# Optimization experiments

Hardware: AMD Instinct MI355X
Metric: run time of the kernel (lower is better)

Reference implementation:

```python
import jax, jax.numpy as jnp
import numpy as np

B, S, D = 2, 2048, 1024   # batch, seq, d_model
E, K, H = 8, 4, 1024      # experts, top-k, expert hidden
SH = 2 * H                # shared-expert hidden (n_shared_experts=2)


def setup_inputs() -> dict:
    key = jax.random.key(0)
    ks = jax.random.split(key, 24)
    f = lambda k, shape: jax.random.normal(k, shape, dtype=jnp.float32) * 0.02
    return {
        "x": jax.random.normal(ks[0], (B, S, D), dtype=jnp.float32),
        # Linear(in_features, out_features), stored as [in, out]
        "lin0_w": f(ks[1], (D, D)), "lin0_b": f(ks[2], (D,)),
        "swi1_w1": f(ks[3], (D, D)), "swi1_b1": f(ks[4], (D,)),
        "swi1_w2": f(ks[5], (D, D)), "swi1_b2": f(ks[6], (D,)),
        # MoE router (no bias) + routed experts (SwiGLU FFN, no bias)
        "gate_w": f(ks[7], (E, D)),
        "exp_w1": f(ks[8], (E, D, H)),
        "exp_w3": f(ks[9], (E, D, H)),
        "exp_w2": f(ks[10], (E, H, D)),
        # shared experts fused into one wider SwiGLU MLP (2 shared experts)
        "sh_w1": f(ks[11], (D, SH)),
        "sh_w3": f(ks[12], (D, SH)),
        "sh_w2": f(ks[13], (SH, D)),
        # second Linear + SwiGLU block (num_ff=2)
        "lin1_w": f(ks[14], (D, D)), "lin1_b": f(ks[15], (D,)),
        "swi2_w1": f(ks[16], (D, D)), "swi2_b1": f(ks[17], (D,)),
        "swi2_w2": f(ks[18], (D, D)), "swi2_b2": f(ks[19], (D,)),
    }


def _silu(x):
    return x * jax.nn.sigmoid(x)


def _swiglu(x, w1, b1, w2, b2):
    return _silu(x @ w1 + b1) * (x @ w2 + b2)


def _moe(x, gate_w, exp_w1, exp_w3, exp_w2, sh_w1, sh_w3, sh_w2):
    b, s, d = x.shape
    t = b * s
    xt = x.reshape(t, d)
    # router: softmax scores, greedy top-k, normalized weights (scaling factor = 1)
    scores = jax.nn.softmax(xt @ gate_w.T, axis=-1)          # [T, E]
    topv, topi = jax.lax.top_k(scores, K)                    # [T, K]
    topv = topv / jnp.sum(topv, axis=-1, keepdims=True)
    combine = jnp.zeros((t, E), xt.dtype).at[jnp.arange(t)[:, None], topi].set(topv)  # [T, E]
    # routed experts: SwiGLU FFN per expert, dense-masked combine (same math as dispatch)
    g = _silu(jnp.einsum('td,edh->eth', xt, exp_w1))
    u = jnp.einsum('td,edh->eth', xt, exp_w3)
    yexp = jnp.einsum('eth,ehd->etd', g * u, exp_w2)         # [E, T, D]
    routed = jnp.einsum('te,etd->td', combine, yexp)         # [T, D]
    # shared experts (always on)
    shared = (_silu(xt @ sh_w1) * (xt @ sh_w3)) @ sh_w2      # [T, D]
    return (routed + shared).reshape(b, s, d)


def reference(x, lin0_w, lin0_b, swi1_w1, swi1_b1, swi1_w2, swi1_b2,
              gate_w, exp_w1, exp_w3, exp_w2, sh_w1, sh_w3, sh_w2,
              lin1_w, lin1_b, swi2_w1, swi2_b1, swi2_w2, swi2_b2):
    h = x @ lin0_w + lin0_b
    h = _swiglu(h, swi1_w1, swi1_b1, swi1_w2, swi1_b2)
    h = _moe(h, gate_w, exp_w1, exp_w3, exp_w2, sh_w1, sh_w3, sh_w2)
    h = h @ lin1_w + lin1_b
    h = _swiglu(h, swi2_w1, swi2_b1, swi2_w2, swi2_b2)
    return h
```

## Files before the change

kernel.cpp:

```cpp
#include <hip/hip_runtime.h>
#include <cstdint>
#include <cstddef>

#define T_TOKENS 4096
#define D_MODEL  1024
#define N_EXP    8
#define TOP_K    4
#define H_EXP    1024
#define SH_HID   2048
#define TK       (T_TOKENS*TOP_K)

typedef __bf16 bf16x8 __attribute__((ext_vector_type(8)));
typedef __bf16 bf16x4 __attribute__((ext_vector_type(4)));
typedef float  f32x4  __attribute__((ext_vector_type(4)));

__device__ __forceinline__ float silu_f(float x) {
    return x / (1.0f + expf(-x));
}

template<int NT, bool SEG, bool GATHER, bool GLU>
__global__ __launch_bounds__(256)
void gemm_sp(const float* __restrict__ A, int lda,
             const float* __restrict__ W1, const float* __restrict__ W3,
             int64_t w_estride, int ldw,
             const float* __restrict__ bias1, const float* __restrict__ bias2,
             float* __restrict__ C, __bf16* __restrict__ Cb1, int ldc,
             int M, int Kd,
             const int* __restrict__ seg_off,
             const int* __restrict__ gather)
{
    constexpr int BM = 128, BN = 128, BK = 32;
    __shared__ __bf16 Asl[NT][BM * BK];
    __shared__ __bf16 Bsl[NT][BN * BK];

    int m0, m1, e = 0;
    if (SEG) {
        e = blockIdx.z;
        int s0 = seg_off[e], s1 = seg_off[e + 1];
        m0 = s0 + blockIdx.y * BM;
        if (m0 >= s1) return;
        m1 = (m0 + BM < s1) ? (m0 + BM) : s1;
    } else {
        m0 = blockIdx.y * BM;
        m1 = (m0 + BM < M) ? (m0 + BM) : M;
    }
    const int n0 = blockIdx.x * BN;

    const int tid  = threadIdx.x;
    const int lane = tid & 63;
    const int w    = tid >> 6;
    const int wm   = w >> 1, wn = w & 1;
    const int fr   = lane & 15, fq = lane >> 4;

    const float* aP[4]; int aR[4], aQ[4];
#pragma unroll
    for (int i = 0; i < 4; ++i) {
        int Li = tid + 256 * i;
        int r = Li >> 3, q = Li & 7;
        aR[i] = r; aQ[i] = q;
        int grow = m0 + r;
        if (grow > m1 - 1) grow = m1 - 1;
        if (GATHER) grow = gather[grow];
        aP[i] = A + (int64_t)grow * lda + q * 4;
    }

    const int bn  = tid & 127;
    const int bkh = tid >> 7;
    const float* Wsrc; int wcol;
    if (GLU) {
        int cl = n0 + bn;
        int B  = cl >> 4;
        Wsrc = (B & 1) ? W3 : W1;
        wcol = ((B >> 1) << 4) | (cl & 15);
    } else {
        Wsrc = W1; wcol = n0 + bn;
    }
    const float* Wb = Wsrc + (int64_t)e * w_estride + (int64_t)(bkh * 16) * ldw + wcol;

    f32x4 zero4 = {0.f, 0.f, 0.f, 0.f};
    f32x4 acc[4][4];
#pragma unroll
    for (int i = 0; i < 4; ++i)
#pragma unroll
        for (int j = 0; j < 4; ++j) acc[i][j] = zero4;

    float4 av[4];
    float  wv[16];

#define GLOADS(K0)                                                         \
    do {                                                                   \
        _Pragma("unroll")                                                  \
        for (int i = 0; i < 4; ++i)                                        \
            av[i] = *reinterpret_cast<const float4*>(aP[i] + (K0));        \
        _Pragma("unroll")                                                  \
        for (int j = 0; j < 16; ++j)                                       \
            wv[j] = Wb[(int64_t)((K0) + j) * ldw];                         \
    } while (0)

    const int nk = Kd / BK;
    GLOADS(0);

    for (int ks = 0; ks < nk; ++ks) {
        bf16x4 pa[NT][4];
        bf16x4 pw[NT][4];
#pragma unroll
        for (int i = 0; i < 4; ++i) {
            float vv[4] = {av[i].x, av[i].y, av[i].z, av[i].w};
#pragma unroll
            for (int t = 0; t < 4; ++t) {
                float v = vv[t];
                __bf16 h = (__bf16)v;
                pa[0][i][t] = h;
                if (NT >= 2) {
                    float r = v - (float)h;
                    if (NT == 2) {
                        pa[1][i][t] = (__bf16)r;
                    } else {
                        __bf16 m = (__bf16)r;
                        pa[1][i][t] = m;
                        pa[2][i][t] = (__bf16)(r - (float)m);
                    }
                }
            }
        }
#pragma unroll
        for (int qd = 0; qd < 4; ++qd) {
#pragma unroll
            for (int t = 0; t < 4; ++t) {
                float v = wv[qd * 4 + t];
                __bf16 h = (__bf16)v;
                pw[0][qd][t] = h;
                if (NT >= 2) {
                    float r = v - (float)h;
                    if (NT == 2) {
                        pw[1][qd][t] = (__bf16)r;
                    } else {
                        __bf16 m = (__bf16)r;
                        pw[1][qd][t] = m;
                        pw[2][qd][t] = (__bf16)(r - (float)m);
                    }
                }
            }
        }

        __syncthreads();
#pragma unroll
        for (int i = 0; i < 4; ++i) {
            int r = aR[i], q = aQ[i];
            int c = (q >> 1) ^ ((r >> 1) & 3);
            int idx = r * BK + c * 8 + (q & 1) * 4;
#pragma unroll
            for (int p = 0; p < NT; ++p)
                *reinterpret_cast<bf16x4*>(&Asl[p][idx]) = pa[p][i];
        }
#pragma unroll
        for (int qd = 0; qd < 4; ++qd) {
            int q32 = bkh * 4 + qd;
            int c = (q32 >> 1) ^ ((bn >> 1) & 3);
            int idx = bn * BK + c * 8 + (q32 & 1) * 4;
#pragma unroll
            for (int p = 0; p < NT; ++p)
                *reinterpret_cast<bf16x4*>(&Bsl[p][idx]) = pw[p][qd];
        }

        if (ks + 1 < nk) GLOADS((ks + 1) * BK);
        __syncthreads();

        bf16x8 bfr[NT][4];
#pragma unroll
        for (int p = 0; p < NT; ++p)
#pragma unroll
            for (int j = 0; j < 4; ++j) {
                int rown = wn * 64 + j * 16 + fr;
                int c = fq ^ ((rown >> 1) & 3);
                bfr[p][j] = *reinterpret_cast<const bf16x8*>(&Bsl[p][rown * BK + c * 8]);
            }
#pragma unroll
        for (int im = 0; im < 4; ++im) {
            bf16x8 af[NT];
            int rowm = wm * 64 + im * 16 + fr;
            int c = fq ^ ((rowm >> 1) & 3);
#pragma unroll
            for (int p = 0; p < NT; ++p)
                af[p] = *reinterpret_cast<const bf16x8*>(&Asl[p][rowm * BK + c * 8]);
#pragma unroll
            for (int jn = 0; jn < 4; ++jn) {
                f32x4 a = acc[im][jn];
                a = __builtin_amdgcn_mfma_f32_16x16x32_bf16(af[0], bfr[0][jn], a, 0, 0, 0);
                if (NT >= 2) {
                    a = __builtin_amdgcn_mfma_f32_16x16x32_bf16(af[0], bfr[1][jn], a, 0, 0, 0);
                    a = __builtin_amdgcn_mfma_f32_16x16x32_bf16(af[1], bfr[0][jn], a, 0, 0, 0);
                }
                if (NT == 3) {
                    a = __builtin_amdgcn_mfma_f32_16x16x32_bf16(af[1], bfr[1][jn], a, 0, 0, 0);
                    a = __builtin_amdgcn_mfma_f32_16x16x32_bf16(af[0], bfr[2][jn], a, 0, 0, 0);
                    a = __builtin_amdgcn_mfma_f32_16x16x32_bf16(af[2], bfr[0][jn], a, 0, 0, 0);
                }
                acc[im][jn] = a;
            }
        }
    }
#undef GLOADS

    if (GLU) {
#pragma unroll
        for (int jn = 0; jn < 4; jn += 2) {
            int gcol = (n0 >> 1) + wn * 32 + (jn >> 1) * 16 + fr;
            float bv1 = bias1 ? bias1[gcol] : 0.f;
            float bv2 = bias2 ? bias2[gcol] : 0.f;
#pragma unroll
            for (int im = 0; im < 4; ++im) {
                f32x4 v1 = acc[im][jn];
                f32x4 v2 = acc[im][jn + 1];
#pragma unroll
                for (int r = 0; r < 4; ++r) {
                    int grow = m0 + wm * 64 + im * 16 + fq * 4 + r;
                    if (grow < m1) {
                        float val = silu_f(v1[r] + bv1) * (v2[r] + bv2);
                        int64_t o = (int64_t)grow * ldc + gcol;
                        C[o] = val;
                        if (Cb1) Cb1[o] = (__bf16)val;
                    }
                }
            }
        }
    } else {
#pragma unroll
        for (int jn = 0; jn < 4; ++jn) {
            int col = n0 + wn * 64 + jn * 16 + fr;
            float bv = bias1 ? bias1[col] : 0.f;
#pragma unroll
            for (int im = 0; im < 4; ++im) {
                f32x4 v = acc[im][jn];
#pragma unroll
                for (int r = 0; r < 4; ++r) {
                    int grow = m0 + wm * 64 + im * 16 + fq * 4 + r;
                    if (grow < m1)
                        C[(int64_t)grow * ldc + col] = v[r] + bv;
                }
            }
        }
    }
}

template<bool WBF, bool SEG, bool GATHER, bool GLU, bool EMITB>
__global__ __launch_bounds__(256)
void gemm_bb(const __bf16* __restrict__ A, int lda,
             const void* __restrict__ W1v, const void* __restrict__ W3v,
             int64_t w_estride, int ldw,
             const float* __restrict__ bias1, const float* __restrict__ bias2,
             float* __restrict__ C, __bf16* __restrict__ Cb, int ldc,
             int M, int Kd,
             const int* __restrict__ seg_off,
             const int* __restrict__ gather)
{
    constexpr int BM = 128, BN = 128, BK = 32;
    __shared__ __bf16 Asl[BM * BK];
    __shared__ __bf16 Bsl[BN * BK];

    int m0, m1, e = 0;
    if (SEG) {
        e = blockIdx.z;
        int s0 = seg_off[e], s1 = seg_off[e + 1];
        m0 = s0 + blockIdx.y * BM;
        if (m0 >= s1) return;
        m1 = (m0 + BM < s1) ? (m0 + BM) : s1;
    } else {
        m0 = blockIdx.y * BM;
        m1 = (m0 + BM < M) ? (m0 + BM) : M;
    }
    const int n0 = blockIdx.x * BN;

    const int tid  = threadIdx.x;
    const int lane = tid & 63;
    const int w    = tid >> 6;
    const int wm   = w >> 1, wn = w & 1;
    const int fr   = lane & 15, fq = lane >> 4;

    int aWr[2]; const __bf16* Ab[2];
#pragma unroll
    for (int i = 0; i < 2; ++i) {
        int L = tid + 256 * i;
        int r = L >> 2, ch = L & 3;
        aWr[i] = r * BK + (ch ^ ((r >> 1) & 3)) * 8;
        int grow = m0 + r;
        if (grow > m1 - 1) grow = m1 - 1;
        if (GATHER) grow = gather[grow];
        Ab[i] = A + (int64_t)grow * lda + ch * 8;
    }

    int wR[2]; const __bf16* Wt[2];
    const float* Wbf = nullptr;
    int wWrS[2];
    if (WBF) {
#pragma unroll
        for (int i = 0; i < 2; ++i) {
            int L = tid + 256 * i;
            int nl = L >> 2, ch = L & 3;
            wR[i] = nl * BK + (ch ^ ((nl >> 1) & 3)) * 8;
            int cl = n0 + nl;
            const __bf16* base;
            int srcrow;
            if (GLU) {
                int B = cl >> 4;
                base = (const __bf16*)((B & 1) ? W3v : W1v);
                srcrow = ((B >> 1) << 4) | (cl & 15);
            } else {
                base = (const __bf16*)W1v;
                srcrow = cl;
            }
            Wt[i] = base + (int64_t)e * w_estride + (int64_t)srcrow * ldw + ch * 8;
        }
    } else {
        const int bn  = tid & 127;
        const int bkh = tid >> 7;
        int wcol; const void* Wsel;
        if (GLU) {
            int cl = n0 + bn;
            int B  = cl >> 4;
            Wsel = (B & 1) ? W3v : W1v;
            wcol = ((B >> 1) << 4) | (cl & 15);
        } else {
            Wsel = W1v; wcol = n0 + bn;
        }
        Wbf = (const float*)Wsel + (int64_t)e * w_estride + (int64_t)(bkh * 16) * ldw + wcol;
#pragma unroll
        for (int c = 0; c < 2; ++c)
            wWrS[c] = bn * BK + ((bkh * 2 + c) ^ ((bn >> 1) & 3)) * 8;
    }

    f32x4 zero4 = {0.f, 0.f, 0.f, 0.f};
    f32x4 acc[4][4];
#pragma unroll
    for (int i = 0; i < 4; ++i)
#pragma unroll
        for (int j = 0; j < 4; ++j) acc[i][j] = zero4;

    bf16x8 areg[2];
    bf16x8 wreg[2];

#define GLOADS(K0)                                                          \
    do {                                                                    \
        areg[0] = *reinterpret_cast<const bf16x8*>(Ab[0] + (K0));           \
        areg[1] = *reinterpret_cast<const bf16x8*>(Ab[1] + (K0));           \
        if (WBF) {                                                          \
            wreg[0] = *reinterpret_cast<const bf16x8*>(Wt[0] + (K0));       \
            wreg[1] = *reinterpret_cast<const bf16x8*>(Wt[1] + (K0));       \
        } else {                                                            \
            _Pragma("unroll")                                               \
            for (int j = 0; j < 16; ++j)                                    \
                wreg[j >> 3][j & 7] = (__bf16)Wbf[(int64_t)((K0) + j) * ldw]; \
        }                                                                   \
    } while (0)

    const int nk = Kd / BK;
    GLOADS(0);

    for (int ks = 0; ks < nk; ++ks) {
        __syncthreads();
        *reinterpret_cast<bf16x8*>(&Asl[aWr[0]]) = areg[0];
        *reinterpret_cast<bf16x8*>(&Asl[aWr[1]]) = areg[1];
        if (WBF) {
            *reinterpret_cast<bf16x8*>(&Bsl[wR[0]]) = wreg[0];
            *reinterpret_cast<bf16x8*>(&Bsl[wR[1]]) = wreg[1];
        } else {
            *reinterpret_cast<bf16x8*>(&Bsl[wWrS[0]]) = wreg[0];
            *reinterpret_cast<bf16x8*>(&Bsl[wWrS[1]]) = wreg[1];
        }
        if (ks + 1 < nk) GLOADS((ks + 1) * BK);
        __syncthreads();

        bf16x8 bfr[4];
#pragma unroll
        for (int j = 0; j < 4; ++j) {
            int rown = wn * 64 + j * 16 + fr;
            int c = fq ^ ((rown >> 1) & 3);
            bfr[j] = *reinterpret_cast<const bf16x8*>(&Bsl[rown * BK + c * 8]);
        }
#pragma unroll
        for (int im = 0; im < 4; ++im) {
            int rowm = wm * 64 + im * 16 + fr;
            int c = fq ^ ((rowm >> 1) & 3);
            bf16x8 af = *reinterpret_cast<const bf16x8*>(&Asl[rowm * BK + c * 8]);
#pragma unroll
            for (int jn = 0; jn < 4; ++jn)
                acc[im][jn] = __builtin_amdgcn_mfma_f32_16x16x32_bf16(af, bfr[jn], acc[im][jn], 0, 0, 0);
        }
    }
#undef GLOADS

    if (GLU) {
#pragma unroll
        for (int jn = 0; jn < 4; jn += 2) {
            int gcol = (n0 >> 1) + wn * 32 + (jn >> 1) * 16 + fr;
            float bv1 = bias1 ? bias1[gcol] : 0.f;
            float bv2 = bias2 ? bias2[gcol] : 0.f;
#pragma unroll
            for (int im = 0; im < 4; ++im) {
                f32x4 v1 = acc[im][jn];
                f32x4 v2 = acc[im][jn + 1];
#pragma unroll
                for (int r = 0; r < 4; ++r) {
                    int grow = m0 + wm * 64 + im * 16 + fq * 4 + r;
                    if (grow < m1) {
                        float val = silu_f(v1[r] + bv1) * (v2[r] + bv2);
                        int64_t o = (int64_t)grow * ldc + gcol;
                        if (EMITB) Cb[o] = (__bf16)val;
                        else       C[o]  = val;
                    }
                }
            }
        }
    } else {
#pragma unroll
        for (int jn = 0; jn < 4; ++jn) {
            int col = n0 + wn * 64 + jn * 16 + fr;
            float bv = bias1 ? bias1[col] : 0.f;
#pragma unroll
            for (int im = 0; im < 4; ++im) {
                f32x4 v = acc[im][jn];
#pragma unroll
                for (int r = 0; r < 4; ++r) {
                    int grow = m0 + wm * 64 + im * 16 + fq * 4 + r;
                    if (grow < m1) {
                        int64_t o = (int64_t)grow * ldc + col;
                        if (EMITB) Cb[o] = (__bf16)(v[r] + bv);
                        else       C[o]  = v[r] + bv;
                    }
                }
            }
        }
    }
}

__global__ __launch_bounds__(256)
void f2bT(const float* __restrict__ src, __bf16* __restrict__ dst, int R, int C)
{
    __shared__ float t[32][33];
    const int64_t eoff = (int64_t)blockIdx.z * R * C;
    src += eoff; dst += eoff;
    const int c0 = blockIdx.x * 32, r0 = blockIdx.y * 32;
    const int tx = threadIdx.x & 31, ty = threadIdx.x >> 5;
#pragma unroll
    for (int i = 0; i < 4; ++i) {
        int r = r0 + ty + i * 8;
        t[ty + i * 8][tx] = src[(int64_t)r * C + c0 + tx];
    }
    __syncthreads();
#pragma unroll
    for (int i = 0; i < 4; ++i) {
        int c = c0 + ty + i * 8;
        dst[(int64_t)c * R + r0 + tx] = (__bf16)t[tx][ty + i * 8];
    }
}

__global__ __launch_bounds__(256)
void router_logits(const float* __restrict__ h1, const float* __restrict__ gw,
                   int* __restrict__ topi, float* __restrict__ topw,
                   unsigned char* __restrict__ emask)
{
    const int wave = threadIdx.x >> 6, lane = threadIdx.x & 63;
    const int t = blockIdx.x * 4 + wave;
    const float* x = h1 + (int64_t)t * D_MODEL;
    float part[N_EXP];
#pragma unroll
    for (int e = 0; e < N_EXP; ++e) part[e] = 0.f;
#pragma unroll 4
    for (int i = 0; i < D_MODEL / 64; ++i) {
        int d = lane + 64 * i;
        float xv = x[d];
#pragma unroll
        for (int e = 0; e < N_EXP; ++e)
            part[e] = fmaf(xv, gw[e * D_MODEL + d], part[e]);
    }
#pragma unroll
    for (int m = 32; m > 0; m >>= 1)
#pragma unroll
        for (int e = 0; e < N_EXP; ++e)
            part[e] += __shfl_xor(part[e], m, 64);

    if (lane == 0) {
        float p[N_EXP];
        float mx = -1e30f;
#pragma unroll
        for (int e = 0; e < N_EXP; ++e) mx = part[e] > mx ? part[e] : mx;
        float z = 0.f;
#pragma unroll
        for (int e = 0; e < N_EXP; ++e) { p[e] = expf(part[e] - mx); z += p[e]; }
#pragma unroll
        for (int e = 0; e < N_EXP; ++e) p[e] /= z;
        bool used[N_EXP];
#pragma unroll
        for (int e = 0; e < N_EXP; ++e) used[e] = false;
        int sel[TOP_K]; float sv[TOP_K]; float wsum = 0.f;
        unsigned m8 = 0;
        for (int k = 0; k < TOP_K; ++k) {
            int best = 0; float bvv = -1.f;
            for (int e = 0; e < N_EXP; ++e)
                if (!used[e] && p[e] > bvv) { bvv = p[e]; best = e; }
            used[best] = true; sel[k] = best; sv[k] = bvv; wsum += bvv;
            m8 |= 1u << best;
        }
        for (int k = 0; k < TOP_K; ++k) {
            int idx = t * TOP_K + k;
            topi[idx] = sel[k];
            topw[idx] = sv[k] / wsum;
        }
        emask[t] = (unsigned char)m8;
    }
}

__global__ __launch_bounds__(256)
void rank_local(const unsigned char* __restrict__ emask,
                const int* __restrict__ topi,
                int* __restrict__ pose, int* __restrict__ bh)
{
    const int b = blockIdx.x;
    const int t = b * 256 + threadIdx.x;
    const int wave = threadIdx.x >> 6, lane = threadIdx.x & 63;
    const unsigned m8 = emask[t];

    __shared__ int wcnt[4][N_EXP];
    __shared__ int wbase[4][N_EXP];
    int lrank[N_EXP];
#pragma unroll
    for (int e = 0; e < N_EXP; ++e) {
        unsigned long long bal = __ballot((m8 >> e) & 1u);
        lrank[e] = __popcll(bal & ((1ull << lane) - 1ull));
        if (lane == 0) wcnt[wave][e] = __popcll(bal);
    }
    __syncthreads();
    if (threadIdx.x < N_EXP) {
        int e = threadIdx.x; int a = 0;
        for (int wv = 0; wv < 4; ++wv) { wbase[wv][e] = a; a += wcnt[wv][e]; }
        bh[b * N_EXP + e] = a;
    }
    __syncthreads();
#pragma unroll
    for (int k = 0; k < TOP_K; ++k) {
        int e = topi[t * TOP_K + k];
        pose[t * TOP_K + k] = wbase[wave][e] + lrank[e];
    }
}

__global__ void scan16(const int* __restrict__ bh, int* __restrict__ bb,
                       int* __restrict__ off)
{
    __shared__ int tot[N_EXP];
    if (threadIdx.x < N_EXP) {
        int e = threadIdx.x; int a = 0;
        for (int b = 0; b < 16; ++b) { bb[b * N_EXP + e] = a; a += bh[b * N_EXP + e]; }
        tot[e] = a;
    }
    __syncthreads();
    if (threadIdx.x == 0) {
        int a = 0; off[0] = 0;
        for (int e = 0; e < N_EXP; ++e) { a += tot[e]; off[e + 1] = a; }
    }
}

__global__ __launch_bounds__(256)
void rank_final(const int* __restrict__ topi, const int* __restrict__ pose,
                const int* __restrict__ bb, const int* __restrict__ off,
                int* __restrict__ perm, int* __restrict__ slot_of)
{
    const int b = blockIdx.x;
    const int t = b * 256 + threadIdx.x;
#pragma unroll
    for (int k = 0; k < TOP_K; ++k) {
        int e = topi[t * TOP_K + k];
        int slot = off[e] + bb[b * N_EXP + e] + pose[t * TOP_K + k];
        perm[slot] = t;
        slot_of[t * TOP_K + k] = slot;
    }
}

template<bool YB>
__global__ __launch_bounds__(256)
void combine_k(const void* __restrict__ yv, const float* __restrict__ topw,
               const int* __restrict__ slot_of, float* __restrict__ h2,
               __bf16* __restrict__ h2b)
{
    int t = blockIdx.x;
    int64_t s[TOP_K]; float wgt[TOP_K];
#pragma unroll
    for (int k = 0; k < TOP_K; ++k) {
        s[k] = slot_of[t * TOP_K + k];
        wgt[k] = topw[t * TOP_K + k];
    }
    int64_t base4 = ((int64_t)t * D_MODEL) / 4 + threadIdx.x;
    float4 v = reinterpret_cast<const float4*>(h2)[base4];
#pragma unroll
    for (int k = 0; k < TOP_K; ++k) {
        float yy[4];
        if (YB) {
            bf16x4 yb = reinterpret_cast<const bf16x4*>((const __bf16*)yv)
                            [s[k] * (D_MODEL / 4) + threadIdx.x];
            yy[0] = (float)yb[0]; yy[1] = (float)yb[1];
            yy[2] = (float)yb[2]; yy[3] = (float)yb[3];
        } else {
            float4 yf = reinterpret_cast<const float4*>((const float*)yv)
                            [s[k] * (D_MODEL / 4) + threadIdx.x];
            yy[0] = yf.x; yy[1] = yf.y; yy[2] = yf.z; yy[3] = yf.w;
        }
        v.x = fmaf(wgt[k], yy[0], v.x);
        v.y = fmaf(wgt[k], yy[1], v.y);
        v.z = fmaf(wgt[k], yy[2], v.z);
        v.w = fmaf(wgt[k], yy[3], v.w);
    }
    if (h2b) {
        bf16x4 o;
        o[0] = (__bf16)v.x; o[1] = (__bf16)v.y;
        o[2] = (__bf16)v.z; o[3] = (__bf16)v.w;
        reinterpret_cast<bf16x4*>(h2b)[base4] = o;
    } else {
        reinterpret_cast<float4*>(h2)[base4] = v;
    }
}

extern "C" void kernel_launch(void* const* d_in, const int* in_sizes, int n_in,
                              void* d_out, int out_size, void* d_ws, size_t ws_size,
                              hipStream_t stream)
{
    const float* x      = (const float*)d_in[0];
    const float* lin0_w = (const float*)d_in[1];
    const float* lin0_b = (const float*)d_in[2];
    const float* s1w1   = (const float*)d_in[3];
    const float* s1b1   = (const float*)d_in[4];
    const float* s1w2   = (const float*)d_in[5];
    const float* s1b2   = (const float*)d_in[6];
    const float* gate_w = (const float*)d_in[7];
    const float* ew1    = (const float*)d_in[8];
    const float* ew3    = (const float*)d_in[9];
    const float* ew2    = (const float*)d_in[10];
    const float* shw1   = (const float*)d_in[11];
    const float* shw3   = (const float*)d_in[12];
    const float* shw2   = (const float*)d_in[13];
    const float* lin1_w = (const float*)d_in[14];
    const float* lin1_b = (const float*)d_in[15];
    const float* s2w1   = (const float*)d_in[16];
    const float* s2b1   = (const float*)d_in[17];
    const float* s2w2   = (const float*)d_in[18];
    const float* s2b2   = (const float*)d_in[19];
    float* out = (float*)d_out;

    char* ws = (char*)d_ws;
    const size_t MB = 1024 * 1024;
    dim3 blk(256);
    const int64_t ES = (int64_t)D_MODEL * H_EXP;
    const bool full = ws_size >= (size_t)216 * MB;

    float* h0 = (float*)(ws + 0 * MB);
    float* h1 = (float*)(ws + 16 * MB);
    float* h2 = (float*)(ws + 32 * MB);

    if (full) {
        __bf16* yexp_b = (__bf16*)(ws + 48 * MB);
        __bf16* gu_b   = (__bf16*)(ws + 80 * MB);
        __bf16* gsh_b  = gu_b;
        __bf16* h1b    = (__bf16*)(ws + 112 * MB);
        __bf16* h2b    = (__bf16*)(ws + 120 * MB);
        __bf16* h3b    = (__bf16*)(ws + 128 * MB);
        __bf16* e1T = (__bf16*)(ws + 136 * MB);
        __bf16* e3T = (__bf16*)(ws + 152 * MB);
        __bf16* e2T = (__bf16*)(ws + 168 * MB);
        __bf16* s1T = (__bf16*)(ws + 184 * MB);
        __bf16* s3T = (__bf16*)(ws + 188 * MB);
        __bf16* s2T = (__bf16*)(ws + 192 * MB);
        __bf16* l1T = (__bf16*)(ws + 196 * MB);
        __bf16* q1T = (__bf16*)(ws + 198 * MB);
        __bf16* q2T = (__bf16*)(ws + 200 * MB);
        char* sm = ws + 202 * MB;
        int*   topi    = (int*)(sm);
        float* topw    = (float*)(sm + 64 * 1024);
        int*   pose    = (int*)(sm + 128 * 1024);
        int*   slot_of = (int*)(sm + 192 * 1024);
        int*   perm    = (int*)(sm + 256 * 1024);
        int*   bh      = (int*)(sm + 320 * 1024);
        int*   bb      = (int*)(sm + 321 * 1024);
        int*   off     = (int*)(sm + 322 * 1024);
        unsigned char* emask = (unsigned char*)(sm + 323 * 1024);

        f2bT<<<dim3(32, 32, N_EXP), blk, 0, stream>>>(ew1, e1T, D_MODEL, H_EXP);
        f2bT<<<dim3(32, 32, N_EXP), blk, 0, stream>>>(ew3, e3T, D_MODEL, H_EXP);
        f2bT<<<dim3(32, 32, N_EXP), blk, 0, stream>>>(ew2, e2T, H_EXP, D_MODEL);
        f2bT<<<dim3(64, 32, 1), blk, 0, stream>>>(shw1, s1T, D_MODEL, SH_HID);
        f2bT<<<dim3(64, 32, 1), blk, 0, stream>>>(shw3, s3T, D_MODEL, SH_HID);
        f2bT<<<dim3(32, 64, 1), blk, 0, stream>>>(shw2, s2T, SH_HID, D_MODEL);
        f2bT<<<dim3(32, 32, 1), blk, 0, stream>>>(lin1_w, l1T, D_MODEL, D_MODEL);
        f2bT<<<dim3(32, 32, 1), blk, 0, stream>>>(s2w1, q1T, D_MODEL, D_MODEL);
        f2bT<<<dim3(32, 32, 1), blk, 0, stream>>>(s2w2, q2T, D_MODEL, D_MODEL);

        gemm_sp<3, false, false, false><<<dim3(8, 32, 1), blk, 0, stream>>>(
            x, D_MODEL, lin0_w, nullptr, 0, D_MODEL, lin0_b, nullptr,
            h0, nullptr, D_MODEL, T_TOKENS, D_MODEL, nullptr, nullptr);

        gemm_sp<3, false, false, true><<<dim3(16, 32, 1), blk, 0, stream>>>(
            h0, D_MODEL, s1w1, s1w2, 0, D_MODEL, s1b1, s1b2,
            h1, h1b, D_MODEL, T_TOKENS, D_MODEL, nullptr, nullptr);

        router_logits<<<T_TOKENS / 4, blk, 0, stream>>>(h1, gate_w, topi, topw, emask);
        rank_local<<<16, blk, 0, stream>>>(emask, topi, pose, bh);
        scan16<<<1, 64, 0, stream>>>(bh, bb, off);
        rank_final<<<16, blk, 0, stream>>>(topi, pose, bb, off, perm, slot_of);

        gemm_bb<true, true, true, true, true><<<dim3(16, 128, N_EXP), blk, 0, stream>>>(
            h1b, D_MODEL, e1T, e3T, ES, D_MODEL, nullptr, nullptr,
            nullptr, gu_b, H_EXP, 0, D_MODEL, off, perm);
        gemm_bb<true, true, false, false, true><<<dim3(8, 128, N_EXP), blk, 0, stream>>>(
            gu_b, H_EXP, e2T, nullptr, ES, H_EXP, nullptr, nullptr,
            nullptr, yexp_b, D_MODEL, 0, H_EXP, off, nullptr);
        gemm_bb<true, false, false, true, true><<<dim3(32, 32, 1), blk, 0, stream>>>(
            h1b, D_MODEL, s1T, s3T, 0, D_MODEL, nullptr, nullptr,
            nullptr, gsh_b, SH_HID, T_TOKENS, D_MODEL, nullptr, nullptr);
        gemm_bb<true, false, false, false, false><<<dim3(8, 32, 1), blk, 0, stream>>>(
            gsh_b, SH_HID, s2T, nullptr, 0, SH_HID, nullptr, nullptr,
            h2, nullptr, D_MODEL, T_TOKENS, SH_HID, nullptr, nullptr);

        combine_k<true><<<T_TOKENS, blk, 0, stream>>>(yexp_b, topw, slot_of, h2, h2b);

        gemm_bb<true, false, false, false, true><<<dim3(8, 32, 1), blk, 0, stream>>>(
            h2b, D_MODEL, l1T, nullptr, 0, D_MODEL, lin1_b, nullptr,
            nullptr, h3b, D_MODEL, T_TOKENS, D_MODEL, nullptr, nullptr);

        gemm_bb<true, false, false, true, false><<<dim3(16, 32, 1), blk, 0, stream>>>(
            h3b, D_MODEL, q1T, q2T, 0, D_MODEL, s2b1, s2b2,
            out, nullptr, D_MODEL, T_TOKENS, D_MODEL, nullptr, nullptr);
    } else {
        float* yexp  = (float*)(ws + 48 * MB);
        __bf16* gu_b = (__bf16*)(ws + 112 * MB);
        __bf16* gsh_b = gu_b;
        __bf16* h1b  = (__bf16*)(ws + 144 * MB);
        char* sm = ws + 152 * MB;
        int*   topi    = (int*)(sm);
        float* topw    = (float*)(sm + 64 * 1024);
        int*   pose    = (int*)(sm + 128 * 1024);
        int*   slot_of = (int*)(sm + 192 * 1024);
        int*   perm    = (int*)(sm + 256 * 1024);
        int*   bh      = (int*)(sm + 320 * 1024);
        int*   bb      = (int*)(sm + 321 * 1024);
        int*   off     = (int*)(sm + 322 * 1024);
        unsigned char* emask = (unsigned char*)(sm + 323 * 1024);

        gemm_sp<3, false, false, false><<<dim3(8, 32, 1), blk, 0, stream>>>(
            x, D_MODEL, lin0_w, nullptr, 0, D_MODEL, lin0_b, nullptr,
            h0, nullptr, D_MODEL, T_TOKENS, D_MODEL, nullptr, nullptr);
        gemm_sp<3, false, false, true><<<dim3(16, 32, 1), blk, 0, stream>>>(
            h0, D_MODEL, s1w1, s1w2, 0, D_MODEL, s1b1, s1b2,
            h1, h1b, D_MODEL, T_TOKENS, D_MODEL, nullptr, nullptr);

        router_logits<<<T_TOKENS / 4, blk, 0, stream>>>(h1, gate_w, topi, topw, emask);
        rank_local<<<16, blk, 0, stream>>>(emask, topi, pose, bh);
        scan16<<<1, 64, 0, stream>>>(bh, bb, off);
        rank_final<<<16, blk, 0, stream>>>(topi, pose, bb, off, perm, slot_of);

        gemm_bb<false, true, true, true, true><<<dim3(16, 128, N_EXP), blk, 0, stream>>>(
            h1b, D_MODEL, ew1, ew3, ES, H_EXP, nullptr, nullptr,
            nullptr, gu_b, H_EXP, 0, D_MODEL, off, perm);
        gemm_bb<false, true, false, false, false><<<dim3(8, 128, N_EXP), blk, 0, stream>>>(
            gu_b, H_EXP, ew2, nullptr, (int64_t)H_EXP * D_MODEL, D_MODEL, nullptr, nullptr,
            yexp, nullptr, D_MODEL, 0, H_EXP, off, nullptr);
        gemm_bb<false, false, false, true, true><<<dim3(32, 32, 1), blk, 0, stream>>>(
            h1b, D_MODEL, shw1, shw3, 0, SH_HID, nullptr, nullptr,
            nullptr, gsh_b, SH_HID, T_TOKENS, D_MODEL, nullptr, nullptr);
        gemm_bb<false, false, false, false, false><<<dim3(8, 32, 1), blk, 0, stream>>>(
            gsh_b, SH_HID, shw2, nullptr, 0, D_MODEL, nullptr, nullptr,
            h2, nullptr, D_MODEL, T_TOKENS, SH_HID, nullptr, nullptr);

        combine_k<false><<<T_TOKENS, blk, 0, stream>>>(yexp, topw, slot_of, h2, nullptr);

        gemm_sp<2, false, false, false><<<dim3(8, 32, 1), blk, 0, stream>>>(
            h2, D_MODEL, lin1_w, nullptr, 0, D_MODEL, lin1_b, nullptr,
            h0, nullptr, D_MODEL, T_TOKENS, D_MODEL, nullptr, nullptr);
        gemm_sp<2, false, false, true><<<dim3(16, 32, 1), blk, 0, stream>>>(
            h0, D_MODEL, s2w1, s2w2, 0, D_MODEL, s2b1, s2b2,
            out, nullptr, D_MODEL, T_TOKENS, D_MODEL, nullptr, nullptr);
    }
}
```

Before: 600.5 us.

## Add double-buffered direct global-to-LDS GEMM for bf16 weight path

Introduces a new GEMM kernel that uses global_load_lds to copy A and W tiles straight into shared memory, bypassing registers. Shared memory is double-buffered so the next K-tile loads while the current one feeds MFMA, with one barrier per iteration instead of two. All bf16-weight GEMM launches in the main path switch to this kernel, and the old bf16-weight branch of gemm_bb is removed. This doubles LDS use per block, which may reduce occupancy, and relies on the per-wave contiguous LDS layout matching the swizzled read pattern.

```diff
diff --git a/kernel.cpp b/kernel.cpp
--- a/kernel.cpp
+++ b/kernel.cpp
@@ -16,6 +16,14 @@
 
 __device__ __forceinline__ float silu_f(float x) {
     return x / (1.0f + expf(-x));
+}
+
+__device__ __forceinline__ void gload16(void* lds, const void* g)
+{
+    __builtin_amdgcn_global_load_lds(
+        (const __attribute__((address_space(1))) unsigned int*)g,
+        (__attribute__((address_space(3))) unsigned int*)lds,
+        16, 0, 0);
 }
 
 template<int NT, bool SEG, bool GATHER, bool GLU>
@@ -243,6 +251,153 @@
     }
 }
 
+template<bool SEG, bool GATHER, bool GLU, bool EMITB>
+__global__ __launch_bounds__(256)
+void gemm_gl(const __bf16* __restrict__ A, int lda,
+             const __bf16* __restrict__ W1, const __bf16* __restrict__ W3,
+             int64_t w_estride, int ldw,
+             const float* __restrict__ bias1, const float* __restrict__ bias2,
+             float* __restrict__ C, __bf16* __restrict__ Cb, int ldc,
+             int M, int Kd,
+             const int* __restrict__ seg_off,
+             const int* __restrict__ gather)
+{
+    constexpr int BK = 32;
+    __shared__ __bf16 Asl[2][128 * BK];
+    __shared__ __bf16 Bsl[2][128 * BK];
+
+    int m0, m1, e = 0;
+    if (SEG) {
+        e = blockIdx.z;
+        int s0 = seg_off[e], s1 = seg_off[e + 1];
+        m0 = s0 + blockIdx.y * 128;
+        if (m0 >= s1) return;
+        m1 = (m0 + 128 < s1) ? (m0 + 128) : s1;
+    } else {
+        m0 = blockIdx.y * 128;
+        m1 = (m0 + 128 < M) ? (m0 + 128) : M;
+    }
+    const int n0 = blockIdx.x * 128;
+
+    const int tid  = threadIdx.x;
+    const int lane = tid & 63;
+    const int w    = tid >> 6;
+    const int wm   = w >> 1, wn = w & 1;
+    const int fr   = lane & 15, fq = lane >> 4;
+
+    const __bf16* As[2]; const __bf16* Ws[2];
+    int ldsOff[2];
+#pragma unroll
+    for (int i = 0; i < 2; ++i) {
+        int L = tid + 256 * i;
+        int r = L >> 2, cp = L & 3;
+        int cs = cp ^ ((r >> 1) & 3);
+        ldsOff[i] = (i * 256 + w * 64) * 8;
+        int grow = m0 + r;
+        if (grow > m1 - 1) grow = m1 - 1;
+        if (GATHER) grow = gather[grow];
+        As[i] = A + (int64_t)grow * lda + cs * 8;
+        int cl = n0 + r;
+        const __bf16* base; int srcrow;
+        if (GLU) {
+            int B = cl >> 4;
+            base = (B & 1) ? W3 : W1;
+            srcrow = ((B >> 1) << 4) | (cl & 15);
+        } else {
+            base = W1; srcrow = cl;
+        }
+        Ws[i] = base + (int64_t)e * w_estride + (int64_t)srcrow * ldw + cs * 8;
+    }
+
+#define STAGE(buf, K0)                                                      \
+    do {                                                                    \
+        _Pragma("unroll")                                                   \
+        for (int i = 0; i < 2; ++i) {                                       \
+            gload16(&Asl[buf][ldsOff[i]], As[i] + (K0));                    \
+            gload16(&Bsl[buf][ldsOff[i]], Ws[i] + (K0));                    \
+        }                                                                   \
+    } while (0)
+
+    f32x4 zero4 = {0.f, 0.f, 0.f, 0.f};
+    f32x4 acc[4][4];
+#pragma unroll
+    for (int i = 0; i < 4; ++i)
+#pragma unroll
+        for (int j = 0; j < 4; ++j) acc[i][j] = zero4;
+
+    const int nk = Kd / BK;
+    int cur = 0;
+    STAGE(0, 0);
+    __syncthreads();
+
+    for (int ks = 0; ks < nk; ++ks) {
+        if (ks + 1 < nk) STAGE(cur ^ 1, (ks + 1) * BK);
+
+        bf16x8 bfr[4];
+#pragma unroll
+        for (int j = 0; j < 4; ++j) {
+            int rown = wn * 64 + j * 16 + fr;
+            int c = fq ^ ((rown >> 1) & 3);
+            bfr[j] = *reinterpret_cast<const bf16x8*>(&Bsl[cur][rown * BK + c * 8]);
+        }
+#pragma unroll
+        for (int im = 0; im < 4; ++im) {
+            int rowm = wm * 64 + im * 16 + fr;
+            int c = fq ^ ((rowm >> 1) & 3);
+            bf16x8 af = *reinterpret_cast<const bf16x8*>(&Asl[cur][rowm * BK + c * 8]);
+#pragma unroll
+            for (int jn = 0; jn < 4; ++jn)
+                acc[im][jn] = __builtin_amdgcn_mfma_f32_16x16x32_bf16(af, bfr[jn], acc[im][jn], 0, 0, 0);
+        }
+        __syncthreads();
+        cur ^= 1;
+    }
+#undef STAGE
+
+    if (GLU) {
+#pragma unroll
+        for (int jn = 0; jn < 4; jn += 2) {
+            int gcol = (n0 >> 1) + wn * 32 + (jn >> 1) * 16 + fr;
+            float bv1 = bias1 ? bias1[gcol] : 0.f;
+            float bv2 = bias2 ? bias2[gcol] : 0.f;
+#pragma unroll
+            for (int im = 0; im < 4; ++im) {
+                f32x4 v1 = acc[im][jn];
+                f32x4 v2 = acc[im][jn + 1];
+#pragma unroll
+                for (int r = 0; r < 4; ++r) {
+                    int grow = m0 + wm * 64 + im * 16 + fq * 4 + r;
+                    if (grow < m1) {
+                        float val = silu_f(v1[r] + bv1) * (v2[r] + bv2);
+                        int64_t o = (int64_t)grow * ldc + gcol;
+                        if (EMITB) Cb[o] = (__bf16)val;
+                        else       C[o]  = val;
+                    }
+                }
+            }
+        }
+    } else {
+#pragma unroll
+        for (int jn = 0; jn < 4; ++jn) {
+            int col = n0 + wn * 64 + jn * 16 + fr;
+            float bv = bias1 ? bias1[col] : 0.f;
+#pragma unroll
+            for (int im = 0; im < 4; ++im) {
+                f32x4 v = acc[im][jn];
+#pragma unroll
+                for (int r = 0; r < 4; ++r) {
+                    int grow = m0 + wm * 64 + im * 16 + fq * 4 + r;
+                    if (grow < m1) {
+                        int64_t o = (int64_t)grow * ldc + col;
+                        if (EMITB) Cb[o] = (__bf16)(v[r] + bv);
+                        else       C[o]  = v[r] + bv;
+                    }
+                }
+            }
+        }
+    }
+}
+
 template<bool WBF, bool SEG, bool GATHER, bool GLU, bool EMITB>
 __global__ __launch_bounds__(256)
 void gemm_bb(const __bf16* __restrict__ A, int lda,
@@ -254,22 +409,22 @@
              const int* __restrict__ seg_off,
              const int* __restrict__ gather)
 {
-    constexpr int BM = 128, BN = 128, BK = 32;
-    __shared__ __bf16 Asl[BM * BK];
-    __shared__ __bf16 Bsl[BN * BK];
+    constexpr int BK = 32;
+    __shared__ __bf16 Asl[128 * BK];
+    __shared__ __bf16 Bsl[128 * BK];
 
     int m0, m1, e = 0;
     if (SEG) {
         e = blockIdx.z;
         int s0 = seg_off[e], s1 = seg_off[e + 1];
-        m0 = s0 + blockIdx.y * BM;
+        m0 = s0 + blockIdx.y * 128;
         if (m0 >= s1) return;
-        m1 = (m0 + BM < s1) ? (m0 + BM) : s1;
+        m1 = (m0 + 128 < s1) ? (m0 + 128) : s1;
     } else {
-        m0 = blockIdx.y * BM;
-        m1 = (m0 + BM < M) ? (m0 + BM) : M;
-    }
-    const int n0 = blockIdx.x * BN;
+        m0 = blockIdx.y * 128;
+        m1 = (m0 + 128 < M) ? (m0 + 128) : M;
+    }
+    const int n0 = blockIdx.x * 128;
 
     const int tid  = threadIdx.x;
     const int lane = tid & 63;
@@ -289,45 +444,22 @@
         Ab[i] = A + (int64_t)grow * lda + ch * 8;
     }
 
-    int wR[2]; const __bf16* Wt[2];
-    const float* Wbf = nullptr;
+    const int bn  = tid & 127;
+    const int bkh = tid >> 7;
+    int wcol; const void* Wsel;
+    if (GLU) {
+        int cl = n0 + bn;
+        int B  = cl >> 4;
+        Wsel = (B & 1) ? W3v : W1v;
+        wcol = ((B >> 1) << 4) | (cl & 15);
+    } else {
+        Wsel = W1v; wcol = n0 + bn;
+    }
+    const float* Wbf = (const float*)Wsel + (int64_t)e * w_estride + (int64_t)(bkh * 16) * ldw + wcol;
     int wWrS[2];
-    if (WBF) {
-#pragma unroll
-        for (int i = 0; i < 2; ++i) {
-            int L = tid + 256 * i;
-            int nl = L >> 2, ch = L & 3;
-            wR[i] = nl * BK + (ch ^ ((nl >> 1) & 3)) * 8;
-            int cl = n0 + nl;
-            const __bf16* base;
-            int srcrow;
-            if (GLU) {
-                int B = cl >> 4;
-                base = (const __bf16*)((B & 1) ? W3v : W1v);
-                srcrow = ((B >> 1) << 4) | (cl & 15);
-            } else {
-                base = (const __bf16*)W1v;
-                srcrow = cl;
-            }
-            Wt[i] = base + (int64_t)e * w_estride + (int64_t)srcrow * ldw + ch * 8;
-        }
-    } else {
-        const int bn  = tid & 127;
-        const int bkh = tid >> 7;
-        int wcol; const void* Wsel;
-        if (GLU) {
-            int cl = n0 + bn;
-            int B  = cl >> 4;
-            Wsel = (B & 1) ? W3v : W1v;
-            wcol = ((B >> 1) << 4) | (cl & 15);
-        } else {
-            Wsel = W1v; wcol = n0 + bn;
-        }
-        Wbf = (const float*)Wsel + (int64_t)e * w_estride + (int64_t)(bkh * 16) * ldw + wcol;
-#pragma unroll
-        for (int c = 0; c < 2; ++c)
-            wWrS[c] = bn * BK + ((bkh * 2 + c) ^ ((bn >> 1) & 3)) * 8;
-    }
+#pragma unroll
+    for (int c = 0; c < 2; ++c)
+        wWrS[c] = bn * BK + ((bkh * 2 + c) ^ ((bn >> 1) & 3)) * 8;
 
     f32x4 zero4 = {0.f, 0.f, 0.f, 0.f};
     f32x4 acc[4][4];
@@ -343,14 +475,9 @@
     do {                                                                    \
         areg[0] = *reinterpret_cast<const bf16x8*>(Ab[0] + (K0));           \
         areg[1] = *reinterpret_cast<const bf16x8*>(Ab[1] + (K0));           \
-        if (WBF) {                                                          \
-            wreg[0] = *reinterpret_cast<const bf16x8*>(Wt[0] + (K0));       \
-            wreg[1] = *reinterpret_cast<const bf16x8*>(Wt[1] + (K0));       \
-        } else {                                                            \
-            _Pragma("unroll")                                               \
-            for (int j = 0; j < 16; ++j)                                    \
-                wreg[j >> 3][j & 7] = (__bf16)Wbf[(int64_t)((K0) + j) * ldw]; \
-        }                                                                   \
+        _Pragma("unroll")                                                   \
+        for (int j = 0; j < 16; ++j)                                        \
+            wreg[j >> 3][j & 7] = (__bf16)Wbf[(int64_t)((K0) + j) * ldw];   \
     } while (0)
 
     const int nk = Kd / BK;
@@ -360,13 +487,8 @@
         __syncthreads();
         *reinterpret_cast<bf16x8*>(&Asl[aWr[0]]) = areg[0];
         *reinterpret_cast<bf16x8*>(&Asl[aWr[1]]) = areg[1];
-        if (WBF) {
-            *reinterpret_cast<bf16x8*>(&Bsl[wR[0]]) = wreg[0];
-            *reinterpret_cast<bf16x8*>(&Bsl[wR[1]]) = wreg[1];
-        } else {
-            *reinterpret_cast<bf16x8*>(&Bsl[wWrS[0]]) = wreg[0];
-            *reinterpret_cast<bf16x8*>(&Bsl[wWrS[1]]) = wreg[1];
-        }
+        *reinterpret_cast<bf16x8*>(&Bsl[wWrS[0]]) = wreg[0];
+        *reinterpret_cast<bf16x8*>(&Bsl[wWrS[1]]) = wreg[1];
         if (ks + 1 < nk) GLOADS((ks + 1) * BK);
         __syncthreads();
 
@@ -704,26 +826,26 @@
         scan16<<<1, 64, 0, stream>>>(bh, bb, off);
         rank_final<<<16, blk, 0, stream>>>(topi, pose, bb, off, perm, slot_of);
 
-        gemm_bb<true, true, true, true, true><<<dim3(16, 128, N_EXP), blk, 0, stream>>>(
+        gemm_gl<true, true, true, true><<<dim3(16, 128, N_EXP), blk, 0, stream>>>(
             h1b, D_MODEL, e1T, e3T, ES, D_MODEL, nullptr, nullptr,
             nullptr, gu_b, H_EXP, 0, D_MODEL, off, perm);
-        gemm_bb<true, true, false, false, true><<<dim3(8, 128, N_EXP), blk, 0, stream>>>(
+        gemm_gl<true, false, false, true><<<dim3(8, 128, N_EXP), blk, 0, stream>>>(
             gu_b, H_EXP, e2T, nullptr, ES, H_EXP, nullptr, nullptr,
             nullptr, yexp_b, D_MODEL, 0, H_EXP, off, nullptr);
-        gemm_bb<true, false, false, true, true><<<dim3(32, 32, 1), blk, 0, stream>>>(
+        gemm_gl<false, false, true, true><<<dim3(32, 32, 1), blk, 0, stream>>>(
             h1b, D_MODEL, s1T, s3T, 0, D_MODEL, nullptr, nullptr,
             nullptr, gsh_b, SH_HID, T_TOKENS, D_MODEL, nullptr, nullptr);
-        gemm_bb<true, false, false, false, false><<<dim3(8, 32, 1), blk, 0, stream>>>(
+        gemm_gl<false, false, false, false><<<dim3(8, 32, 1), blk, 0, stream>>>(
             gsh_b, SH_HID, s2T, nullptr, 0, SH_HID, nullptr, nullptr,
             h2, nullptr, D_MODEL, T_TOKENS, SH_HID, nullptr, nullptr);
 
         combine_k<true><<<T_TOKENS, blk, 0, stream>>>(yexp_b, topw, slot_of, h2, h2b);
 
-        gemm_bb<true, false, false, false, true><<<dim3(8, 32, 1), blk, 0, stream>>>(
+        gemm_gl<false, false, false, true><<<dim3(8, 32, 1), blk, 0, stream>>>(
             h2b, D_MODEL, l1T, nullptr, 0, D_MODEL, lin1_b, nullptr,
             nullptr, h3b, D_MODEL, T_TOKENS, D_MODEL, nullptr, nullptr);
 
-        gemm_bb<true, false, false, true, false><<<dim3(16, 32, 1), blk, 0, stream>>>(
+        gemm_gl<false, false, true, false><<<dim3(16, 32, 1), blk, 0, stream>>>(
             h3b, D_MODEL, q1T, q2T, 0, D_MODEL, s2b1, s2b2,
             out, nullptr, D_MODEL, T_TOKENS, D_MODEL, nullptr, nullptr);
     } else {
```

After: 609.6 us. About the same (+1.5%).
